# Kernel tuning notes

Measured on AMD Instinct MI355X. Metric: run time of the kernel, lower is better.

The kernel has to match this reference:

```python
import jax, jax.numpy as jnp
import numpy as np

DIM = 512
HID = 4 * DIM
EPS = 1e-5


def _layernorm(x, g, b):
    mu = jnp.mean(x, axis=-1, keepdims=True)
    var = jnp.mean(jnp.square(x - mu), axis=-1, keepdims=True)
    return (x - mu) * jax.lax.rsqrt(var + EPS) * g + b


def setup_inputs() -> dict:
    key = jax.random.key(0)
    ks = jax.random.split(key, 16)
    s = 1.0 / np.sqrt(DIM)
    sh = 1.0 / np.sqrt(HID)
    inp = {
        "x": jax.random.normal(ks[0], (4, 4096, DIM), dtype=jnp.float32),
        "ln1_g": jnp.ones((DIM,), jnp.float32),
        "ln1_b": jnp.zeros((DIM,), jnp.float32),
        "Wq": jax.random.normal(ks[1], (DIM, DIM), jnp.float32) * s,
        "bq": jnp.zeros((DIM,), jnp.float32),
        "Wk": jax.random.normal(ks[2], (DIM, DIM), jnp.float32) * s,
        "bk": jnp.zeros((DIM,), jnp.float32),
        "Wv": jax.random.normal(ks[3], (DIM, DIM), jnp.float32) * s,
        "bv": jnp.zeros((DIM,), jnp.float32),
        "Wo": jax.random.normal(ks[4], (DIM, DIM), jnp.float32) * s,
        "bo": jnp.zeros((DIM,), jnp.float32),
        "ln2_g": jnp.ones((DIM,), jnp.float32),
        "ln2_b": jnp.zeros((DIM,), jnp.float32),
        "W1": jax.random.normal(ks[5], (DIM, HID), jnp.float32) * s,
        "b1": jnp.zeros((HID,), jnp.float32),
        "W2": jax.random.normal(ks[6], (HID, DIM), jnp.float32) * sh,
        "b2": jnp.zeros((DIM,), jnp.float32),
    }
    return inp


def reference(x, ln1_g, ln1_b, Wq, bq, Wk, bk, Wv, bv, Wo, bo, ln2_g, ln2_b, W1, b1, W2, b2):
    # Pre-norm self attention (single head, naive softmax(QK^T)V)
    h = _layernorm(x, ln1_g, ln1_b)
    q = h @ Wq + bq  # [B,S,D]
    k = h @ Wk + bk
    v = h @ Wv + bv
    scale = q.shape[-1] ** (-0.5)
    scores = jnp.einsum("bsd,btd->bst", q, k) * scale  # [B,S,S]
    attn = jax.nn.softmax(scores, axis=-1)
    o = jnp.einsum("bst,btd->bsd", attn, v) @ Wo + bo
    x = x + o
    # Pre-norm GELU MLP (exact erf gelu, matching torch F.gelu default)
    h2 = _layernorm(x, ln2_g, ln2_b)
    m = jax.nn.gelu(h2 @ W1 + b1, approximate=False) @ W2 + b2
    return x + m
```

## Files before the change

kernel.cpp:

```cpp
#include <hip/hip_runtime.h>

typedef unsigned short u16;
typedef float f32x4 __attribute__((ext_vector_type(4)));
typedef __bf16 bf16x8 __attribute__((ext_vector_type(8)));

__device__ __forceinline__ u16 f2bf(float f) {
  unsigned u = __float_as_uint(f);
  u += 0x7fffu + ((u >> 16) & 1u);
  return (u16)(u >> 16);
}

__device__ __forceinline__ f32x4 mfma16(bf16x8 a, bf16x8 b, f32x4 c) {
  return __builtin_amdgcn_mfma_f32_16x16x32_bf16(a, b, c, 0, 0, 0);
}

#define GLDS16(gp, lp)                                                            \
  __builtin_amdgcn_global_load_lds((const __attribute__((address_space(1))) void*)(gp), \
                                   (__attribute__((address_space(3))) void*)(lp), 16, 0, 0)

__global__ __launch_bounds__(256) void prep_all(const float* __restrict__ Wq,
                                                const float* __restrict__ Wk,
                                                const float* __restrict__ Wv,
                                                const float* __restrict__ Wo,
                                                const float* __restrict__ W1,
                                                const float* __restrict__ W2,
                                                u16* __restrict__ Wqkvt, u16* __restrict__ Wot,
                                                u16* __restrict__ W1t, u16* __restrict__ W2t) {
  __shared__ float t[32][33];
  const int bid = blockIdx.x;
  const float* in;
  u16* out;
  int R, C, bx, by;
  if (bid < 256) {
    in = Wq; out = Wqkvt; R = 512; C = 512; bx = bid & 15; by = bid >> 4;
  } else if (bid < 512) {
    in = Wk; out = Wqkvt + 262144; R = 512; C = 512; bx = (bid - 256) & 15; by = (bid - 256) >> 4;
  } else if (bid < 768) {
    in = Wv; out = Wqkvt + 524288; R = 512; C = 512; bx = (bid - 512) & 15; by = (bid - 512) >> 4;
  } else if (bid < 1024) {
    in = Wo; out = Wot; R = 512; C = 512; bx = (bid - 768) & 15; by = (bid - 768) >> 4;
  } else if (bid < 2048) {
    in = W1; out = W1t; R = 512; C = 2048; bx = (bid - 1024) & 63; by = (bid - 1024) >> 6;
  } else {
    in = W2; out = W2t; R = 2048; C = 512; bx = (bid - 2048) & 15; by = (bid - 2048) >> 4;
  }
  const int c0 = bx * 32, r0 = by * 32;
  const int tx = threadIdx.x & 31, ty = threadIdx.x >> 5;
#pragma unroll
  for (int j = 0; j < 4; ++j)
    t[ty * 4 + j][tx] = in[(size_t)(r0 + ty * 4 + j) * C + c0 + tx];
  __syncthreads();
#pragma unroll
  for (int j = 0; j < 4; ++j)
    out[(size_t)(c0 + ty * 4 + j) * R + r0 + tx] = f2bf(t[tx][ty * 4 + j]);
}

__global__ __launch_bounds__(256) void ln_fwd(const float* __restrict__ x,
                                              const float* __restrict__ gw,
                                              const float* __restrict__ bw,
                                              u16* __restrict__ out) {
  int row = blockIdx.x * 4 + (threadIdx.x >> 6);
  int lane = threadIdx.x & 63;
  const float* xr = x + (size_t)row * 512;
  float xv[8], gv[8], bv[8];
  *(float4*)&xv[0] = *(const float4*)(xr + lane * 8);
  *(float4*)&xv[4] = *(const float4*)(xr + lane * 8 + 4);
  *(float4*)&gv[0] = *(const float4*)(gw + lane * 8);
  *(float4*)&gv[4] = *(const float4*)(gw + lane * 8 + 4);
  *(float4*)&bv[0] = *(const float4*)(bw + lane * 8);
  *(float4*)&bv[4] = *(const float4*)(bw + lane * 8 + 4);
  float sum = 0.f, sq = 0.f;
#pragma unroll
  for (int j = 0; j < 8; ++j) { sum += xv[j]; sq += xv[j] * xv[j]; }
#pragma unroll
  for (int d = 1; d < 64; d <<= 1) {
    sum += __shfl_xor(sum, d);
    sq += __shfl_xor(sq, d);
  }
  float mean = sum * (1.f / 512.f);
  float var = sq * (1.f / 512.f) - mean * mean;
  float rstd = rsqrtf(var + 1e-5f);
  union { uint4 u; u16 h[8]; } ob;
#pragma unroll
  for (int j = 0; j < 8; ++j)
    ob.h[j] = f2bf((xv[j] - mean) * rstd * gv[j] + bv[j]);
  *(uint4*)(out + (size_t)row * 512 + lane * 8) = ob.u;
}

template <int EPI>
__global__ __launch_bounds__(256, 2) void gemm_bt(const u16* __restrict__ A, int lda, size_t sA,
                                                  const u16* __restrict__ Bt, int ldb, size_t sB,
                                                  const float* __restrict__ bias,
                                                  const float* __restrict__ bias1,
                                                  const float* __restrict__ bias2,
                                                  const float* __restrict__ res,
                                                  u16* __restrict__ vtg,
                                                  void* __restrict__ out, int ldc, size_t sC,
                                                  int M, int N, int K) {
  __shared__ u16 As[128 * 64];
  __shared__ u16 Bs[128 * 64];
  const int tid = threadIdx.x;
  const int lane = tid & 63, w = tid >> 6;
  const int wr = w >> 1, wc = w & 1;
  const int m0 = blockIdx.x * 128, n0 = blockIdx.y * 128;
  const int lh = lane >> 4, ll = lane & 15;
  A += (size_t)blockIdx.z * sA;
  Bt += (size_t)blockIdx.z * sB;

  const int srow = lane >> 2;
  const int scol = (lane & 3) * 8;
  const u16* ga = A + (size_t)(m0 + srow) * lda + scol;
  const u16* gb = Bt + (size_t)(n0 + srow) * ldb + scol;

  bf16x8 ones;
#pragma unroll
  for (int j = 0; j < 8; ++j) ones[j] = (__bf16)1.0f;

  f32x4 acc[4][4] = {};
  f32x4 accs[4] = {};
  const int nk = K >> 6;
  for (int kt = 0; kt < nk; ++kt) {
    const int k0 = kt << 6;
#pragma unroll
    for (int j = 0; j < 4; ++j) {
      const int t = w * 4 + j;
      const int radd = (t & 7) * 16;
      const int kadd = (t >> 3) * 32;
      GLDS16(ga + (size_t)radd * lda + k0 + kadd, &As[t * 512]);
      GLDS16(gb + (size_t)radd * ldb + k0 + kadd, &Bs[t * 512]);
    }
    __syncthreads();
#pragma unroll
    for (int ks = 0; ks < 2; ++ks) {
      bf16x8 a[4], b[4];
#pragma unroll
      for (int m = 0; m < 4; ++m)
        a[m] = *(const bf16x8*)&As[ks * 4096 + (wr * 64 + m * 16 + ll) * 32 + lh * 8];
#pragma unroll
      for (int n = 0; n < 4; ++n)
        b[n] = *(const bf16x8*)&Bs[ks * 4096 + (wc * 64 + n * 16 + ll) * 32 + lh * 8];
#pragma unroll
      for (int m = 0; m < 4; ++m)
#pragma unroll
        for (int n = 0; n < 4; ++n)
          acc[m][n] = mfma16(a[m], b[n], acc[m][n]);
      if (EPI == 4) {
#pragma unroll
        for (int m = 0; m < 4; ++m) accs[m] = mfma16(a[m], ones, accs[m]);
      }
    }
    __syncthreads();
  }

  u16* outh = (u16*)out + (size_t)blockIdx.z * sC;
  float* outf = (float*)out + (size_t)blockIdx.z * sC;
#pragma unroll
  for (int m = 0; m < 4; ++m) {
    int row = m0 + wr * 64 + m * 16 + lh * 4;
#pragma unroll
    for (int n = 0; n < 4; ++n) {
      int col = n0 + wc * 64 + n * 16 + ll;
      float bv = 0.f;
      if (EPI == 1) {
        const float* bp = (col < 512) ? bias : (col < 1024 ? bias1 : bias2);
        bv = bp[col & 511];
      } else if (EPI == 2 || EPI == 3) {
        bv = bias[col];
      }
      if (EPI == 1 && col >= 1024) {
        union { uint2 u; u16 h[4]; } pk;
#pragma unroll
        for (int i = 0; i < 4; ++i) pk.h[i] = f2bf(acc[m][n][i] + bv);
        const int b = row >> 12, brow = row & 4095;
        *(uint2*)&vtg[((size_t)(b * 512 + (col - 1024))) * 4096 + brow] = pk.u;
      } else {
#pragma unroll
        for (int i = 0; i < 4; ++i) {
          float v = acc[m][n][i] + bv;
          size_t idx = (size_t)(row + i) * ldc + col;
          if (EPI == 2) {
            float y = 0.7978845608028654f * (v + 0.044715f * v * v * v);
            v = v / (1.f + __expf(-2.f * y));
          }
          if (EPI == 4) v = v * (1.f / accs[m][i]);
          if (EPI == 5) v = __expf(v * 0.044194173824159216f);
          if (EPI == 3)
            outf[idx] = v + res[(size_t)blockIdx.z * sC + idx];
          else
            outh[idx] = f2bf(v);
        }
      }
    }
  }
}

extern "C" void kernel_launch(void* const* d_in, const int* in_sizes, int n_in,
                              void* d_out, int out_size, void* d_ws, size_t ws_size,
                              hipStream_t stream) {
  const float* x     = (const float*)d_in[0];
  const float* ln1g  = (const float*)d_in[1];
  const float* ln1b  = (const float*)d_in[2];
  const float* Wq    = (const float*)d_in[3];
  const float* bq    = (const float*)d_in[4];
  const float* Wk    = (const float*)d_in[5];
  const float* bk    = (const float*)d_in[6];
  const float* Wv    = (const float*)d_in[7];
  const float* bVv   = (const float*)d_in[8];
  const float* Wo    = (const float*)d_in[9];
  const float* bo    = (const float*)d_in[10];
  const float* ln2g  = (const float*)d_in[11];
  const float* ln2b  = (const float*)d_in[12];
  const float* W1    = (const float*)d_in[13];
  const float* b1    = (const float*)d_in[14];
  const float* W2    = (const float*)d_in[15];
  const float* b2    = (const float*)d_in[16];

  char* base = (char*)d_ws;
  u16* Wqkvt = (u16*)base;
  u16* Wot   = Wqkvt + 786432;
  u16* W1t   = Wot + 262144;
  u16* W2t   = W1t + 1048576;
  u16* qkvb = (u16*)(base + (8ull << 20));
  u16* Vt   = qkvb + (size_t)16384 * 1536;
  u16* m1   = qkvb;
  u16* hb   = (u16*)(base + (72ull << 20));
  const size_t sco_off = 88ull << 20;
  u16* scores = (u16*)(base + sco_off);
  float* x1 = (float*)scores;

  const size_t S = 4096;
  const size_t per_b = S * S * 2;
  int nb = 1;
  if (ws_size >= sco_off + 4 * per_b) nb = 4;
  else if (ws_size >= sco_off + 2 * per_b) nb = 2;

  prep_all<<<3072, 256, 0, stream>>>(Wq, Wk, Wv, Wo, W1, W2, Wqkvt, Wot, W1t, W2t);

  ln_fwd<<<4096, 256, 0, stream>>>(x, ln1g, ln1b, hb);
  gemm_bt<1><<<dim3(128, 12, 1), 256, 0, stream>>>(hb, 512, 0, Wqkvt, 512, 0,
                                                   bq, bk, bVv, nullptr, Vt,
                                                   qkvb, 1536, 0, 16384, 1536, 512);

  for (int b0 = 0; b0 < 4; b0 += nb) {
    int nz = (4 - b0) < nb ? (4 - b0) : nb;
    const u16* qk = qkvb + (size_t)b0 * S * 1536;
    gemm_bt<5><<<dim3(32, 32, nz), 256, 0, stream>>>(qk, 1536, S * 1536, qk + 512, 1536, S * 1536,
                                                     nullptr, nullptr, nullptr, nullptr, nullptr,
                                                     scores, 4096, S * S, 4096, 4096, 512);
    gemm_bt<4><<<dim3(32, 4, nz), 256, 0, stream>>>(scores, 4096, S * S,
                                                    Vt + (size_t)b0 * 512 * S, 4096, 512 * S,
                                                    nullptr, nullptr, nullptr, nullptr, nullptr,
                                                    hb + (size_t)b0 * S * 512, 512, S * 512,
                                                    4096, 512, 4096);
  }

  gemm_bt<3><<<dim3(128, 4, 1), 256, 0, stream>>>(hb, 512, 0, Wot, 512, 0,
                                                  bo, nullptr, nullptr, x, nullptr,
                                                  x1, 512, 0, 16384, 512, 512);
  ln_fwd<<<4096, 256, 0, stream>>>(x1, ln2g, ln2b, hb);
  gemm_bt<2><<<dim3(128, 16, 1), 256, 0, stream>>>(hb, 512, 0, W1t, 512, 0,
                                                   b1, nullptr, nullptr, nullptr, nullptr,
                                                   m1, 2048, 0, 16384, 2048, 512);
  gemm_bt<3><<<dim3(128, 4, 1), 256, 0, stream>>>(m1, 2048, 0, W2t, 2048, 0,
                                                  b2, nullptr, nullptr, x1, nullptr,
                                                  (float*)d_out, 512, 0, 16384, 512, 2048);
}
```

Measured before the change: 352.9 us.

## Fuse softmax row sums into score GEMM epilogue and add XCD block swizzle

The exp-score GEMM now reduces each row's bf16-rounded exp values across its tile and writes per-tile partial sums to a workspace buffer. The PV GEMM reads and combines these partials instead of running extra MFMAs against a ones vector every k-step. Separately, a template flag remaps block IDs round-robin across 8 groups, presumably to match the MI355X's XCD layout and improve L2 locality. The changes add workspace traffic and an extra barrier in the score epilogue, and rely on the psum region not overlapping other buffers.

After: 381.1 us. +8.0%, slower.

```diff
diff --git a/kernel.cpp b/kernel.cpp
--- a/kernel.cpp
+++ b/kernel.cpp
@@ -87,7 +87,7 @@
   *(uint4*)(out + (size_t)row * 512 + lane * 8) = ob.u;
 }
 
-template <int EPI>
+template <int EPI, int SWZ>
 __global__ __launch_bounds__(256, 2) void gemm_bt(const u16* __restrict__ A, int lda, size_t sA,
                                                   const u16* __restrict__ Bt, int ldb, size_t sB,
                                                   const float* __restrict__ bias,
@@ -95,29 +95,51 @@
                                                   const float* __restrict__ bias2,
                                                   const float* __restrict__ res,
                                                   u16* __restrict__ vtg,
+                                                  float* __restrict__ psum,
                                                   void* __restrict__ out, int ldc, size_t sC,
                                                   int M, int N, int K) {
   __shared__ u16 As[128 * 64];
   __shared__ u16 Bs[128 * 64];
+  __shared__ float rowtmp[256];
   const int tid = threadIdx.x;
   const int lane = tid & 63, w = tid >> 6;
   const int wr = w >> 1, wc = w & 1;
-  const int m0 = blockIdx.x * 128, n0 = blockIdx.y * 128;
   const int lh = lane >> 4, ll = lane & 15;
-  A += (size_t)blockIdx.z * sA;
-  Bt += (size_t)blockIdx.z * sB;
+
+  int bx = blockIdx.x, by = blockIdx.y, bz = blockIdx.z;
+  if (SWZ) {
+    const int gx = gridDim.x, gy = gridDim.y;
+    const int nwg = gx * gy * gridDim.z;
+    const int lid = bx + gx * (by + gy * bz);
+    const int cpx = nwg >> 3;
+    const int s = (lid & 7) * cpx + (lid >> 3);
+    bx = s % gx;
+    const int r2 = s / gx;
+    by = r2 % gy;
+    bz = r2 / gy;
+  }
+  const int m0 = bx * 128, n0 = by * 128;
+  A += (size_t)bz * sA;
+  Bt += (size_t)bz * sB;
 
   const int srow = lane >> 2;
   const int scol = (lane & 3) * 8;
   const u16* ga = A + (size_t)(m0 + srow) * lda + scol;
   const u16* gb = Bt + (size_t)(n0 + srow) * ldb + scol;
 
-  bf16x8 ones;
-#pragma unroll
-  for (int j = 0; j < 8; ++j) ones[j] = (__bf16)1.0f;
+  float psacc = 0.f;
+  if (EPI == 4) {
+    const float* pp = psum + ((size_t)bz * 4096 + m0 + (tid >> 1)) * 32 + (tid & 1) * 16;
+    float4 p0 = *(const float4*)pp;
+    float4 p1 = *(const float4*)(pp + 4);
+    float4 p2 = *(const float4*)(pp + 8);
+    float4 p3 = *(const float4*)(pp + 12);
+    psacc = ((p0.x + p0.y) + (p0.z + p0.w)) + ((p1.x + p1.y) + (p1.z + p1.w)) +
+            ((p2.x + p2.y) + (p2.z + p2.w)) + ((p3.x + p3.y) + (p3.z + p3.w));
+    rowtmp[tid] = psacc;
+  }
 
   f32x4 acc[4][4] = {};
-  f32x4 accs[4] = {};
   const int nk = K >> 6;
   for (int kt = 0; kt < nk; ++kt) {
     const int k0 = kt << 6;
@@ -144,19 +166,30 @@
 #pragma unroll
         for (int n = 0; n < 4; ++n)
           acc[m][n] = mfma16(a[m], b[n], acc[m][n]);
-      if (EPI == 4) {
-#pragma unroll
-        for (int m = 0; m < 4; ++m) accs[m] = mfma16(a[m], ones, accs[m]);
+    }
+    __syncthreads();
+  }
+
+  u16* outh = (u16*)out + (size_t)bz * sC;
+  float* outf = (float*)out + (size_t)bz * sC;
+  float rs[4][4];
+  if (EPI == 5) {
+#pragma unroll
+    for (int m = 0; m < 4; ++m)
+#pragma unroll
+      for (int i = 0; i < 4; ++i) rs[m][i] = 0.f;
+  }
+#pragma unroll
+  for (int m = 0; m < 4; ++m) {
+    int row = m0 + wr * 64 + m * 16 + lh * 4;
+    float invv[4];
+    if (EPI == 4) {
+#pragma unroll
+      for (int i = 0; i < 4; ++i) {
+        int rl = wr * 64 + m * 16 + lh * 4 + i;
+        invv[i] = 1.f / (rowtmp[rl * 2] + rowtmp[rl * 2 + 1]);
       }
     }
-    __syncthreads();
-  }
-
-  u16* outh = (u16*)out + (size_t)blockIdx.z * sC;
-  float* outf = (float*)out + (size_t)blockIdx.z * sC;
-#pragma unroll
-  for (int m = 0; m < 4; ++m) {
-    int row = m0 + wr * 64 + m * 16 + lh * 4;
 #pragma unroll
     for (int n = 0; n < 4; ++n) {
       int col = n0 + wc * 64 + n * 16 + ll;
@@ -182,15 +215,37 @@
             float y = 0.7978845608028654f * (v + 0.044715f * v * v * v);
             v = v / (1.f + __expf(-2.f * y));
           }
-          if (EPI == 4) v = v * (1.f / accs[m][i]);
-          if (EPI == 5) v = __expf(v * 0.044194173824159216f);
-          if (EPI == 3)
-            outf[idx] = v + res[(size_t)blockIdx.z * sC + idx];
-          else
+          if (EPI == 4) v = v * invv[i];
+          if (EPI == 5) {
+            v = __expf(v * 0.044194173824159216f);
+            u16 h = f2bf(v);
+            outh[idx] = h;
+            rs[m][i] += __uint_as_float((unsigned)h << 16);
+          } else if (EPI == 3) {
+            outf[idx] = v + res[(size_t)bz * sC + idx];
+          } else {
             outh[idx] = f2bf(v);
+          }
         }
       }
     }
+  }
+  if (EPI == 5) {
+    float* sumlds = (float*)As;
+#pragma unroll
+    for (int m = 0; m < 4; ++m)
+#pragma unroll
+      for (int i = 0; i < 4; ++i) {
+        float r = rs[m][i];
+        r += __shfl_xor(r, 1);
+        r += __shfl_xor(r, 2);
+        r += __shfl_xor(r, 4);
+        r += __shfl_xor(r, 8);
+        if (ll == 0) sumlds[wc * 128 + wr * 64 + m * 16 + lh * 4 + i] = r;
+      }
+    __syncthreads();
+    if (tid < 128)
+      psum[((size_t)bz * 4096 + m0 + tid) * 32 + by] = sumlds[tid] + sumlds[128 + tid];
   }
 }
 
@@ -220,6 +275,7 @@
   u16* Wot   = Wqkvt + 786432;
   u16* W1t   = Wot + 262144;
   u16* W2t   = W1t + 1048576;
+  float* psum = (float*)(base + 6291456ull);
   u16* qkvb = (u16*)(base + (8ull << 20));
   u16* Vt   = qkvb + (size_t)16384 * 1536;
   u16* m1   = qkvb;
@@ -237,31 +293,31 @@
   prep_all<<<3072, 256, 0, stream>>>(Wq, Wk, Wv, Wo, W1, W2, Wqkvt, Wot, W1t, W2t);
 
   ln_fwd<<<4096, 256, 0, stream>>>(x, ln1g, ln1b, hb);
-  gemm_bt<1><<<dim3(128, 12, 1), 256, 0, stream>>>(hb, 512, 0, Wqkvt, 512, 0,
-                                                   bq, bk, bVv, nullptr, Vt,
-                                                   qkvb, 1536, 0, 16384, 1536, 512);
+  gemm_bt<1, 1><<<dim3(128, 12, 1), 256, 0, stream>>>(hb, 512, 0, Wqkvt, 512, 0,
+                                                      bq, bk, bVv, nullptr, Vt, nullptr,
+                                                      qkvb, 1536, 0, 16384, 1536, 512);
 
   for (int b0 = 0; b0 < 4; b0 += nb) {
     int nz = (4 - b0) < nb ? (4 - b0) : nb;
     const u16* qk = qkvb + (size_t)b0 * S * 1536;
-    gemm_bt<5><<<dim3(32, 32, nz), 256, 0, stream>>>(qk, 1536, S * 1536, qk + 512, 1536, S * 1536,
-                                                     nullptr, nullptr, nullptr, nullptr, nullptr,
-                                                     scores, 4096, S * S, 4096, 4096, 512);
-    gemm_bt<4><<<dim3(32, 4, nz), 256, 0, stream>>>(scores, 4096, S * S,
-                                                    Vt + (size_t)b0 * 512 * S, 4096, 512 * S,
-                                                    nullptr, nullptr, nullptr, nullptr, nullptr,
-                                                    hb + (size_t)b0 * S * 512, 512, S * 512,
-                                                    4096, 512, 4096);
-  }
-
-  gemm_bt<3><<<dim3(128, 4, 1), 256, 0, stream>>>(hb, 512, 0, Wot, 512, 0,
-                                                  bo, nullptr, nullptr, x, nullptr,
-                                                  x1, 512, 0, 16384, 512, 512);
+    gemm_bt<5, 1><<<dim3(32, 32, nz), 256, 0, stream>>>(qk, 1536, S * 1536, qk + 512, 1536, S * 1536,
+                                                        nullptr, nullptr, nullptr, nullptr, nullptr,
+                                                        psum, scores, 4096, S * S, 4096, 4096, 512);
+    gemm_bt<4, 0><<<dim3(32, 4, nz), 256, 0, stream>>>(scores, 4096, S * S,
+                                                       Vt + (size_t)b0 * 512 * S, 4096, 512 * S,
+                                                       nullptr, nullptr, nullptr, nullptr, nullptr,
+                                                       psum, hb + (size_t)b0 * S * 512, 512, S * 512,
+                                                       4096, 512, 4096);
+  }
+
+  gemm_bt<3, 0><<<dim3(128, 4, 1), 256, 0, stream>>>(hb, 512, 0, Wot, 512, 0,
+                                                     bo, nullptr, nullptr, x, nullptr, nullptr,
+                                                     x1, 512, 0, 16384, 512, 512);
   ln_fwd<<<4096, 256, 0, stream>>>(x1, ln2g, ln2b, hb);
-  gemm_bt<2><<<dim3(128, 16, 1), 256, 0, stream>>>(hb, 512, 0, W1t, 512, 0,
-                                                   b1, nullptr, nullptr, nullptr, nullptr,
-                                                   m1, 2048, 0, 16384, 2048, 512);
-  gemm_bt<3><<<dim3(128, 4, 1), 256, 0, stream>>>(m1, 2048, 0, W2t, 2048, 0,
-                                                  b2, nullptr, nullptr, x1, nullptr,
-                                                  (float*)d_out, 512, 0, 16384, 512, 2048);
-}
+  gemm_bt<2, 1><<<dim3(128, 16, 1), 256, 0, stream>>>(hb, 512, 0, W1t, 512, 0,
+                                                      b1, nullptr, nullptr, nullptr, nullptr, nullptr,
+                                                      m1, 2048, 0, 16384, 2048, 512);
+  gemm_bt<3, 0><<<dim3(128, 4, 1), 256, 0, stream>>>(m1, 2048, 0, W2t, 2048, 0,
+                                                     b2, nullptr, nullptr, x1, nullptr, nullptr,
+                                                     (float*)d_out, 512, 0, 16384, 512, 2048);
+}
```

## Add 256x128-tile 512-thread GEMM with XCD-aware block swizzle for large GEMMs

Applied to the files above, without the earlier changes.

Introduces a gemm_bt256 kernel with 256-row tiles and 8 waves per block, used for the QKV projection, the QK^T score GEMM and the W1 MLP GEMM. It adds a block index remap that spreads consecutive workgroups across the eight XCDs for better L2 locality. The original kernel is slimmed to only the EPI 3/4 epilogues. Bigger tiles cut B-operand reloads per output, at the cost of more LDS per block and possibly lower occupancy.

Result: slower. 380.8 us (+7.9%).

```diff
diff --git a/kernel.cpp b/kernel.cpp
--- a/kernel.cpp
+++ b/kernel.cpp
@@ -91,10 +91,7 @@
 __global__ __launch_bounds__(256, 2) void gemm_bt(const u16* __restrict__ A, int lda, size_t sA,
                                                   const u16* __restrict__ Bt, int ldb, size_t sB,
                                                   const float* __restrict__ bias,
-                                                  const float* __restrict__ bias1,
-                                                  const float* __restrict__ bias2,
                                                   const float* __restrict__ res,
-                                                  u16* __restrict__ vtg,
                                                   void* __restrict__ out, int ldc, size_t sC,
                                                   int M, int N, int K) {
   __shared__ u16 As[128 * 64];
@@ -160,11 +157,103 @@
 #pragma unroll
     for (int n = 0; n < 4; ++n) {
       int col = n0 + wc * 64 + n * 16 + ll;
+      float bv = (EPI == 3) ? bias[col] : 0.f;
+#pragma unroll
+      for (int i = 0; i < 4; ++i) {
+        float v = acc[m][n][i] + bv;
+        size_t idx = (size_t)(row + i) * ldc + col;
+        if (EPI == 4) v = v * (1.f / accs[m][i]);
+        if (EPI == 3)
+          outf[idx] = v + res[(size_t)blockIdx.z * sC + idx];
+        else
+          outh[idx] = f2bf(v);
+      }
+    }
+  }
+}
+
+template <int EPI, int SWZ>
+__global__ __launch_bounds__(512, 2) void gemm_bt256(const u16* __restrict__ A, int lda, size_t sA,
+                                                     const u16* __restrict__ Bt, int ldb, size_t sB,
+                                                     const float* __restrict__ bias,
+                                                     const float* __restrict__ bias1,
+                                                     const float* __restrict__ bias2,
+                                                     u16* __restrict__ vtg,
+                                                     void* __restrict__ out, int ldc, size_t sC,
+                                                     int M, int N, int K) {
+  __shared__ u16 As[256 * 64];
+  __shared__ u16 Bs[128 * 64];
+  const int tid = threadIdx.x;
+  const int lane = tid & 63, w = tid >> 6;
+  const int wr = w >> 1, wc = w & 1;
+  const int lh = lane >> 4, ll = lane & 15;
+
+  int bx = blockIdx.x, by = blockIdx.y, bz = blockIdx.z;
+  if (SWZ) {
+    const int gx = gridDim.x, gy = gridDim.y;
+    const int nwg = gx * gy * gridDim.z;
+    const int lid = bx + gx * (by + gy * bz);
+    const int cpx = nwg >> 3;
+    const int s = (lid & 7) * cpx + (lid >> 3);
+    bx = s % gx;
+    const int r2 = s / gx;
+    by = r2 % gy;
+    bz = r2 / gy;
+  }
+  const int m0 = bx * 256, n0 = by * 128;
+  A += (size_t)bz * sA;
+  Bt += (size_t)bz * sB;
+
+  const int srow = lane >> 2;
+  const int scol = (lane & 3) * 8;
+  const u16* ga = A + (size_t)(m0 + srow) * lda + scol;
+  const u16* gb = Bt + (size_t)(n0 + srow) * ldb + scol;
+
+  f32x4 acc[4][4] = {};
+  const int nk = K >> 6;
+  for (int kt = 0; kt < nk; ++kt) {
+    const int k0 = kt << 6;
+#pragma unroll
+    for (int j = 0; j < 4; ++j) {
+      const int t = w * 4 + j;
+      GLDS16(ga + (size_t)((t & 15) * 16) * lda + k0 + (t >> 4) * 32, &As[t * 512]);
+    }
+#pragma unroll
+    for (int j = 0; j < 2; ++j) {
+      const int t2 = w * 2 + j;
+      GLDS16(gb + (size_t)((t2 & 7) * 16) * ldb + k0 + (t2 >> 3) * 32, &Bs[t2 * 512]);
+    }
+    __syncthreads();
+#pragma unroll
+    for (int ks = 0; ks < 2; ++ks) {
+      bf16x8 a[4], b[4];
+#pragma unroll
+      for (int m = 0; m < 4; ++m)
+        a[m] = *(const bf16x8*)&As[ks * 8192 + (wr * 64 + m * 16 + ll) * 32 + lh * 8];
+#pragma unroll
+      for (int n = 0; n < 4; ++n)
+        b[n] = *(const bf16x8*)&Bs[ks * 4096 + (wc * 64 + n * 16 + ll) * 32 + lh * 8];
+#pragma unroll
+      for (int m = 0; m < 4; ++m)
+#pragma unroll
+        for (int n = 0; n < 4; ++n)
+          acc[m][n] = mfma16(a[m], b[n], acc[m][n]);
+    }
+    __syncthreads();
+  }
+
+  u16* outh = (u16*)out + (size_t)bz * sC;
+#pragma unroll
+  for (int m = 0; m < 4; ++m) {
+    int row = m0 + wr * 64 + m * 16 + lh * 4;
+#pragma unroll
+    for (int n = 0; n < 4; ++n) {
+      int col = n0 + wc * 64 + n * 16 + ll;
       float bv = 0.f;
       if (EPI == 1) {
         const float* bp = (col < 512) ? bias : (col < 1024 ? bias1 : bias2);
         bv = bp[col & 511];
-      } else if (EPI == 2 || EPI == 3) {
+      } else if (EPI == 2) {
         bv = bias[col];
       }
       if (EPI == 1 && col >= 1024) {
@@ -182,12 +271,8 @@
             float y = 0.7978845608028654f * (v + 0.044715f * v * v * v);
             v = v / (1.f + __expf(-2.f * y));
           }
-          if (EPI == 4) v = v * (1.f / accs[m][i]);
           if (EPI == 5) v = __expf(v * 0.044194173824159216f);
-          if (EPI == 3)
-            outf[idx] = v + res[(size_t)blockIdx.z * sC + idx];
-          else
-            outh[idx] = f2bf(v);
+          outh[idx] = f2bf(v);
         }
       }
     }
@@ -237,31 +322,30 @@
   prep_all<<<3072, 256, 0, stream>>>(Wq, Wk, Wv, Wo, W1, W2, Wqkvt, Wot, W1t, W2t);
 
   ln_fwd<<<4096, 256, 0, stream>>>(x, ln1g, ln1b, hb);
-  gemm_bt<1><<<dim3(128, 12, 1), 256, 0, stream>>>(hb, 512, 0, Wqkvt, 512, 0,
-                                                   bq, bk, bVv, nullptr, Vt,
-                                                   qkvb, 1536, 0, 16384, 1536, 512);
+  gemm_bt256<1, 1><<<dim3(64, 12, 1), 512, 0, stream>>>(hb, 512, 0, Wqkvt, 512, 0,
+                                                        bq, bk, bVv, Vt,
+                                                        qkvb, 1536, 0, 16384, 1536, 512);
 
   for (int b0 = 0; b0 < 4; b0 += nb) {
     int nz = (4 - b0) < nb ? (4 - b0) : nb;
     const u16* qk = qkvb + (size_t)b0 * S * 1536;
-    gemm_bt<5><<<dim3(32, 32, nz), 256, 0, stream>>>(qk, 1536, S * 1536, qk + 512, 1536, S * 1536,
-                                                     nullptr, nullptr, nullptr, nullptr, nullptr,
-                                                     scores, 4096, S * S, 4096, 4096, 512);
+    gemm_bt256<5, 1><<<dim3(16, 32, nz), 512, 0, stream>>>(qk, 1536, S * 1536,
+                                                           qk + 512, 1536, S * 1536,
+                                                           nullptr, nullptr, nullptr, nullptr,
+                                                           scores, 4096, S * S, 4096, 4096, 512);
     gemm_bt<4><<<dim3(32, 4, nz), 256, 0, stream>>>(scores, 4096, S * S,
                                                     Vt + (size_t)b0 * 512 * S, 4096, 512 * S,
-                                                    nullptr, nullptr, nullptr, nullptr, nullptr,
+                                                    nullptr, nullptr,
                                                     hb + (size_t)b0 * S * 512, 512, S * 512,
                                                     4096, 512, 4096);
   }
 
-  gemm_bt<3><<<dim3(128, 4, 1), 256, 0, stream>>>(hb, 512, 0, Wot, 512, 0,
-                                                  bo, nullptr, nullptr, x, nullptr,
+  gemm_bt<3><<<dim3(128, 4, 1), 256, 0, stream>>>(hb, 512, 0, Wot, 512, 0, bo, x,
                                                   x1, 512, 0, 16384, 512, 512);
   ln_fwd<<<4096, 256, 0, stream>>>(x1, ln2g, ln2b, hb);
-  gemm_bt<2><<<dim3(128, 16, 1), 256, 0, stream>>>(hb, 512, 0, W1t, 512, 0,
-                                                   b1, nullptr, nullptr, nullptr, nullptr,
-                                                   m1, 2048, 0, 16384, 2048, 512);
-  gemm_bt<3><<<dim3(128, 4, 1), 256, 0, stream>>>(m1, 2048, 0, W2t, 2048, 0,
-                                                  b2, nullptr, nullptr, x1, nullptr,
+  gemm_bt256<2, 1><<<dim3(64, 16, 1), 512, 0, stream>>>(hb, 512, 0, W1t, 512, 0,
+                                                        b1, nullptr, nullptr, nullptr,
+                                                        m1, 2048, 0, 16384, 2048, 512);
+  gemm_bt<3><<<dim3(128, 4, 1), 256, 0, stream>>>(m1, 2048, 0, W2t, 2048, 0, b2, x1,
                                                   (float*)d_out, 512, 0, 16384, 512, 2048);
 }
```
